# Kernel tuning notes

Measured on AMD Instinct MI355X. Metric: run time of the kernel, lower is better.

Reference implementation:

```python
import jax, jax.numpy as jnp
import numpy as np

N_HEAD = 16
NEG_INF = -1e30  # finite mask value, safe for softmax/grad


def setup_inputs() -> dict:
    key = jax.random.key(0)
    k1, k2, k3 = jax.random.split(key, 3)
    B, T, C = 4, 2049, 1024
    x = jax.random.normal(k1, (B, T, C), dtype=jnp.float32)
    W_attn = jax.random.normal(k2, (C, 3 * C), dtype=jnp.float32) * (1.0 / np.sqrt(C))
    W_proj = jax.random.normal(k3, (C, C), dtype=jnp.float32) * (1.0 / np.sqrt(C))
    return {"x": x, "W_attn": W_attn, "W_proj": W_proj}


def reference(x, W_attn, W_proj):
    B, T, C = x.shape
    H = N_HEAD
    D = C // H
    qkv = x @ W_attn                                  # (B, T, 3C)
    q, k, v = jnp.split(qkv, 3, axis=-1)
    q = q.reshape(B, T, H, D).transpose(0, 2, 1, 3)   # (B, H, T, D)
    k = k.reshape(B, T, H, D).transpose(0, 2, 1, 3)
    v = v.reshape(B, T, H, D).transpose(0, 2, 1, 3)
    # hybrid mask: causal tril, but state token (row 0) attends to ALL positions
    mask = jnp.tril(jnp.ones((T, T), dtype=bool))
    mask = mask.at[0, :].set(True)
    scale = 1.0 / np.sqrt(D)
    scores = jnp.einsum('bhtd,bhsd->bhts', q, k) * scale
    scores = jnp.where(mask[None, None, :, :], scores, NEG_INF)
    att = jax.nn.softmax(scores, axis=-1)
    y = jnp.einsum('bhts,bhsd->bhtd', att, v)         # (B, H, T, D)
    y = y.transpose(0, 2, 1, 3).reshape(B, T, C)
    return y @ W_proj
```

## Files before the change

### kernel.cpp

```cpp
#include <hip/hip_runtime.h>

typedef __attribute__((ext_vector_type(8))) __bf16 bf16x8;
typedef __attribute__((ext_vector_type(4))) __bf16 bf16x4;
typedef __attribute__((ext_vector_type(4))) float f32x4;
typedef __attribute__((ext_vector_type(16))) float f32x16;

#define GLDS(g, l) __builtin_amdgcn_global_load_lds( \
    (__attribute__((address_space(1))) void*)(void*)(g), \
    (__attribute__((address_space(3))) void*)(void*)(l), 16, 0, 0)

constexpr int T_REAL = 2049;
constexpr int Tp     = 2112;
constexpr int Mreal  = 8196;
constexpr int Mp     = 8448;
constexpr int GK     = 1024;

constexpr float QSCALE = 0.125f * 1.4426950408889634f;

__global__ __launch_bounds__(256) void cvt_x(const float* __restrict__ x,
                                             __bf16* __restrict__ xb) {
    size_t i = ((size_t)blockIdx.x * 256 + threadIdx.x) * 4;
    float4 v = make_float4(0.f, 0.f, 0.f, 0.f);
    if (i < (size_t)Mreal * GK) v = *(const float4*)(x + i);
    bf16x4 o;
    o.x = (__bf16)v.x; o.y = (__bf16)v.y; o.z = (__bf16)v.z; o.w = (__bf16)v.w;
    *(bf16x4*)(xb + i) = o;
}

__global__ __launch_bounds__(256) void transpose_w(const float* __restrict__ W,
                                                   __bf16* __restrict__ Wt,
                                                   int K, int N) {
    __shared__ float tile[64][65];
    const int n0 = blockIdx.x * 64, k0 = blockIdx.y * 64;
    const int tx = threadIdx.x & 63, ty = threadIdx.x >> 6;
#pragma unroll
    for (int j = 0; j < 16; j++) {
        int rk = ty + j * 4;
        tile[rk][tx] = W[(size_t)(k0 + rk) * N + n0 + tx];
    }
    __syncthreads();
#pragma unroll
    for (int j = 0; j < 16; j++) {
        int rn = ty + j * 4;
        Wt[(size_t)(n0 + rn) * K + k0 + tx] = (__bf16)tile[tx][rn];
    }
}

__global__ __launch_bounds__(256) void transpose_v(const __bf16* __restrict__ v,
                                                   __bf16* __restrict__ vT) {
    __shared__ __bf16 tl[64][72];
    const int bh = blockIdx.y, t0 = blockIdx.x * 64;
    const int tid = threadIdx.x;
    const __bf16* src = v + ((size_t)bh * Tp + t0) * 64;
    {
        const int r = tid >> 3, c = (tid & 7) * 8;
        *(bf16x8*)&tl[r][c]      = *(const bf16x8*)(src + r * 64 + c);
        *(bf16x8*)&tl[r + 32][c] = *(const bf16x8*)(src + (r + 32) * 64 + c);
    }
    __syncthreads();
    __bf16* dst = vT + (size_t)bh * 64 * Tp + t0;
    {
        const int d = tid >> 3, tc = (tid & 7) * 8;
        bf16x8 a, b;
#pragma unroll
        for (int i = 0; i < 8; i++) {
            a[i] = tl[tc + i][d];
            b[i] = tl[tc + i][d + 32];
        }
        *(bf16x8*)(dst + (size_t)d * Tp + tc)        = a;
        *(bf16x8*)(dst + (size_t)(d + 32) * Tp + tc) = b;
    }
}

__global__ __launch_bounds__(512)
void gemm256(const __bf16* __restrict__ A, const __bf16* __restrict__ Bt,
             __bf16* __restrict__ qout, __bf16* __restrict__ kout,
             __bf16* __restrict__ vout) {
    __shared__ __align__(16) __bf16 As[2][16384];
    __shared__ __align__(16) __bf16 Bs[2][16384];

    const int tid = threadIdx.x, lane = tid & 63, w = tid >> 6;
    const int wr = w >> 2, wc = w & 3;
    const int quad = lane >> 4, l15 = lane & 15, l7 = l15 & 7;
    const int m0 = blockIdx.y * 256, n0 = blockIdx.x * 256;

    const int sr = tid >> 3;
    const int sc = ((tid & 7) ^ (sr & 7)) * 8;
    const __bf16* ag = A  + (size_t)(m0 + sr) * GK + sc;
    const __bf16* bg = Bt + (size_t)(n0 + sr) * GK + sc;
    const int ldst = tid * 8;

#define STG_A(T, h) do { const __bf16* s_ = ag + (size_t)(h) * 128 * GK + (T) * 64; \
    GLDS(s_, &As[(T) & 1][(h) * 8192 + ldst]); \
    GLDS(s_ + (size_t)64 * GK, &As[(T) & 1][(h) * 8192 + 4096 + ldst]); } while (0)
#define STG_B(T, h) do { const __bf16* s_ = bg + (size_t)(h) * 128 * GK + (T) * 64; \
    GLDS(s_, &Bs[(T) & 1][(h) * 8192 + ldst]); \
    GLDS(s_ + (size_t)64 * GK, &Bs[(T) & 1][(h) * 8192 + 4096 + ldst]); } while (0)

    f32x4 acc[8][4] = {};
    bf16x8 a[8], b0[4], b1[4];

    STG_A(0, 0); STG_B(0, 1); STG_A(0, 1); STG_B(0, 0); STG_A(1, 0); STG_B(1, 1);
    asm volatile("s_waitcnt vmcnt(4)" ::: "memory");
    __builtin_amdgcn_s_barrier();

    constexpr int NT = GK / 64;

#pragma unroll 1
    for (int T = 0; T < NT; ++T) {
        const int p = T & 1;

#pragma unroll
        for (int f = 0; f < 4; ++f) {
            const int R = f * 32 + wr * 16 + l15;
            a[f * 2 + 0] = *(const bf16x8*)&As[p][R * 64 + ((quad ^ l7) * 8)];
            a[f * 2 + 1] = *(const bf16x8*)&As[p][R * 64 + (((4 + quad) ^ l7) * 8)];
        }
#pragma unroll
        for (int n = 0; n < 2; ++n) {
            const int R = n * 64 + wc * 16 + l15;
            b0[n * 2 + 0] = *(const bf16x8*)&Bs[p][R * 64 + ((quad ^ l7) * 8)];
            b0[n * 2 + 1] = *(const bf16x8*)&Bs[p][R * 64 + (((4 + quad) ^ l7) * 8)];
        }
        if (T + 1 < NT) { STG_A(T + 1, 1); STG_B(T + 1, 0); }
        __builtin_amdgcn_s_barrier();
        asm volatile("s_waitcnt lgkmcnt(0)" ::: "memory");
        __builtin_amdgcn_sched_barrier(0);
        __builtin_amdgcn_s_setprio(1);
#pragma unroll
        for (int f = 0; f < 4; ++f)
#pragma unroll
            for (int n = 0; n < 2; ++n) {
                acc[f][n] = __builtin_amdgcn_mfma_f32_16x16x32_bf16(a[f*2+0], b0[n*2+0], acc[f][n], 0, 0, 0);
                acc[f][n] = __builtin_amdgcn_mfma_f32_16x16x32_bf16(a[f*2+1], b0[n*2+1], acc[f][n], 0, 0, 0);
            }
        __builtin_amdgcn_s_setprio(0);
        __builtin_amdgcn_s_barrier();

#pragma unroll
        for (int n = 0; n < 2; ++n) {
            const int R = 128 + n * 64 + wc * 16 + l15;
            b1[n * 2 + 0] = *(const bf16x8*)&Bs[p][R * 64 + ((quad ^ l7) * 8)];
            b1[n * 2 + 1] = *(const bf16x8*)&Bs[p][R * 64 + (((4 + quad) ^ l7) * 8)];
        }
        __builtin_amdgcn_s_barrier();
        asm volatile("s_waitcnt lgkmcnt(0)" ::: "memory");
        __builtin_amdgcn_sched_barrier(0);
        __builtin_amdgcn_s_setprio(1);
#pragma unroll
        for (int f = 0; f < 4; ++f)
#pragma unroll
            for (int n = 0; n < 2; ++n) {
                acc[f][2+n] = __builtin_amdgcn_mfma_f32_16x16x32_bf16(a[f*2+0], b1[n*2+0], acc[f][2+n], 0, 0, 0);
                acc[f][2+n] = __builtin_amdgcn_mfma_f32_16x16x32_bf16(a[f*2+1], b1[n*2+1], acc[f][2+n], 0, 0, 0);
            }
        __builtin_amdgcn_s_setprio(0);
        __builtin_amdgcn_s_barrier();

#pragma unroll
        for (int f = 0; f < 4; ++f) {
            const int R = 128 + f * 32 + wr * 16 + l15;
            a[f * 2 + 0] = *(const bf16x8*)&As[p][R * 64 + ((quad ^ l7) * 8)];
            a[f * 2 + 1] = *(const bf16x8*)&As[p][R * 64 + (((4 + quad) ^ l7) * 8)];
        }
        if (T + 2 < NT) STG_A(T + 2, 0);
        __builtin_amdgcn_s_barrier();
        asm volatile("s_waitcnt lgkmcnt(0)" ::: "memory");
        __builtin_amdgcn_sched_barrier(0);
        __builtin_amdgcn_s_setprio(1);
#pragma unroll
        for (int f = 0; f < 4; ++f)
#pragma unroll
            for (int n = 0; n < 2; ++n) {
                acc[4+f][2+n] = __builtin_amdgcn_mfma_f32_16x16x32_bf16(a[f*2+0], b1[n*2+0], acc[4+f][2+n], 0, 0, 0);
                acc[4+f][2+n] = __builtin_amdgcn_mfma_f32_16x16x32_bf16(a[f*2+1], b1[n*2+1], acc[4+f][2+n], 0, 0, 0);
            }
        __builtin_amdgcn_s_setprio(0);
        __builtin_amdgcn_s_barrier();

        if (T + 2 < NT) STG_B(T + 2, 1);
        __builtin_amdgcn_s_barrier();
        asm volatile("s_waitcnt lgkmcnt(0)" ::: "memory");
        __builtin_amdgcn_sched_barrier(0);
        __builtin_amdgcn_s_setprio(1);
#pragma unroll
        for (int f = 0; f < 4; ++f)
#pragma unroll
            for (int n = 0; n < 2; ++n) {
                acc[4+f][n] = __builtin_amdgcn_mfma_f32_16x16x32_bf16(a[f*2+0], b0[n*2+0], acc[4+f][n], 0, 0, 0);
                acc[4+f][n] = __builtin_amdgcn_mfma_f32_16x16x32_bf16(a[f*2+1], b0[n*2+1], acc[4+f][n], 0, 0, 0);
            }
        __builtin_amdgcn_s_setprio(0);
        if (T < NT - 2) { asm volatile("s_waitcnt vmcnt(4)" ::: "memory"); }
        else            { asm volatile("s_waitcnt vmcnt(0)" ::: "memory"); }
        __builtin_amdgcn_s_barrier();
    }
#undef STG_A
#undef STG_B

    const int which = n0 >> 10;
    __bf16* op = (which == 0) ? qout : (which == 1) ? kout : vout;
    const float scl = (which == 0) ? QSCALE : 1.0f;
    __bf16* ep = &As[0][0];
    const int rr = tid >> 4, cc = tid & 15;
#pragma unroll
    for (int f = 0; f < 8; ++f) {
        __syncthreads();
#pragma unroll
        for (int n = 0; n < 4; ++n) {
            const int col = (n & 1) * 64 + wc * 16 + (n >> 1) * 128 + l15;
#pragma unroll
            for (int r = 0; r < 4; ++r)
                ep[(wr * 16 + quad * 4 + r) * 264 + col] = (__bf16)(acc[f][n][r] * scl);
        }
        __syncthreads();
        const int m = m0 + (f & 3) * 32 + (f >> 2) * 128 + rr;
        if (m < Mreal) {
            const int b = m / T_REAL;
            const int t = m - b * T_REAL;
#pragma unroll
            for (int g = 0; g < 2; ++g) {
                const int c8 = (cc + g * 16) * 8;
                bf16x8 vv = *(const bf16x8*)&ep[rr * 264 + c8];
                const int gc = n0 + c8;
                const int h = (gc >> 6) & 15;
                *(bf16x8*)&op[((size_t)(b * 16 + h) * Tp + t) * 64 + (gc & 63)] = vv;
            }
        }
    }
}

template <int EPI>
__global__ __launch_bounds__(256)
void gemm128(const __bf16* __restrict__ A, const __bf16* __restrict__ Bt,
             float* __restrict__ outp,
             __bf16* __restrict__ qout, __bf16* __restrict__ kout,
             __bf16* __restrict__ vout) {
    __shared__ __bf16 As[128 * 64];
    __shared__ __bf16 Bs[128 * 64];

    const int tid = threadIdx.x, lane = tid & 63, w = tid >> 6;
    const int wr = w >> 1, wc = w & 1;
    const int quad = lane >> 4, l15 = lane & 15, l7 = l15 & 7;
    const int m0 = blockIdx.y * 128, n0 = blockIdx.x * 128;

    const int row0 = w * 32 + (lane >> 3);
    const int gc8 = ((lane & 7) ^ ((lane >> 3) & 7)) * 8;
    const __bf16* agp = A + (size_t)(m0 + row0) * GK + gc8;
    const __bf16* bgp = Bt + (size_t)(n0 + row0) * GK + gc8;
    __bf16* lap = &As[(w * 256 + lane) * 8];
    __bf16* lbp = &Bs[(w * 256 + lane) * 8];

    f32x4 acc[4][4] = {};

    for (int k0 = 0; k0 < GK; k0 += 64) {
#pragma unroll
        for (int s = 0; s < 4; s++) {
            GLDS(agp + (size_t)s * 8 * GK + k0, lap + s * 512);
            GLDS(bgp + (size_t)s * 8 * GK + k0, lbp + s * 512);
        }
        __syncthreads();
#pragma unroll
        for (int kk = 0; kk < 2; kk++) {
            bf16x8 fa[4], fb[4];
#pragma unroll
            for (int i = 0; i < 4; i++)
                fa[i] = *(const bf16x8*)&As[(wr * 64 + i * 16 + l15) * 64 + (((kk * 4 + quad) ^ l7) * 8)];
#pragma unroll
            for (int j = 0; j < 4; j++)
                fb[j] = *(const bf16x8*)&Bs[(wc * 64 + j * 16 + l15) * 64 + (((kk * 4 + quad) ^ l7) * 8)];
#pragma unroll
            for (int i = 0; i < 4; i++)
#pragma unroll
                for (int j = 0; j < 4; j++)
                    acc[i][j] = __builtin_amdgcn_mfma_f32_16x16x32_bf16(fa[i], fb[j], acc[i][j], 0, 0, 0);
        }
        __syncthreads();
    }

    if constexpr (EPI == 0) {
        const int which = n0 >> 10;
        const int h = ((n0 + wc * 64) >> 6) & 15;
        __bf16* op = (which == 0) ? qout : (which == 1) ? kout : vout;
        const float scl = (which == 0) ? QSCALE : 1.0f;
        __bf16* wls = &As[w * 2048];
#pragma unroll
        for (int p = 0; p < 2; p++) {
            if (p) __syncthreads();
#pragma unroll
            for (int i2 = 0; i2 < 2; i2++)
#pragma unroll
                for (int j = 0; j < 4; j++)
#pragma unroll
                    for (int r = 0; r < 4; r++) {
                        const int lrow = i2 * 16 + quad * 4 + r;
                        const int cX = (j * 2 + (l15 >> 3)) ^ (lrow & 7);
                        wls[lrow * 64 + cX * 8 + (l15 & 7)] =
                            (__bf16)(acc[p * 2 + i2][j][r] * scl);
                    }
            __syncthreads();
#pragma unroll
            for (int it = 0; it < 4; it++) {
                const int lrow = (lane >> 3) + it * 8;
                bf16x8 vv = *(const bf16x8*)&wls[lrow * 64 + (((lane & 7) ^ (lrow & 7)) * 8)];
                const int m = m0 + wr * 64 + p * 32 + lrow;
                if (m < Mreal) {
                    const int b = m / T_REAL;
                    const int t = m - b * T_REAL;
                    *(bf16x8*)&op[(((size_t)(b * 16 + h)) * Tp + t) * 64 + (lane & 7) * 8] = vv;
                }
            }
        }
    } else {
        float* wlf = (float*)&As[0] + w * 1024;
#pragma unroll
        for (int p = 0; p < 4; p++) {
            if (p) __syncthreads();
#pragma unroll
            for (int j = 0; j < 4; j++)
#pragma unroll
                for (int r = 0; r < 4; r++) {
                    const int lrow = quad * 4 + r;
                    const int cX = (j * 4 + (l15 >> 2)) ^ (lrow & 7);
                    wlf[lrow * 64 + cX * 4 + (l15 & 3)] = acc[p][j][r];
                }
            __syncthreads();
#pragma unroll
            for (int it = 0; it < 4; it++) {
                const int lrow = lane >> 2;
                const int c = (lane & 3) + it * 4;
                f32x4 vv = *(const f32x4*)&wlf[lrow * 64 + ((c ^ (lrow & 7)) * 4)];
                const int m = m0 + wr * 64 + p * 16 + lrow;
                if (m < Mreal)
                    *(f32x4*)&outp[(size_t)m * 1024 + n0 + wc * 64 + c * 4] = vv;
            }
        }
    }
}

__global__ __launch_bounds__(256, 4)
void attn(const __bf16* __restrict__ q, const __bf16* __restrict__ kk,
          const __bf16* __restrict__ vT, __bf16* __restrict__ y) {
    __shared__ __bf16 Ks[2][64 * 64];
    __shared__ __bf16 Vs[2][64 * 64];

    static const int QA[17] = {0,31,29,27,25,23,21,19,17,15,13,11,9,7,5,3,1};
    static const int QB[17] = {32,30,28,26,24,22,20,18,16,14,12,10,8,6,4,2,-1};

    const int tid = threadIdx.x, lane = tid & 63, w = tid >> 6;
    const int l31 = lane & 31, hi = lane >> 5, l7 = l31 & 7;
    const int z = blockIdx.x;
    const int slot = z >> 6, zz = z & 63;
    const int bh = (zz & 7) * 8 + (zz >> 3);

    const int qtA = QA[slot];
    const int qt = (w < 2) ? qtA : QB[slot];
    const bool active = qt >= 0;
    const int qts = active ? qt : 0;
    const int qg = qts * 64 + (w & 1) * 32 + l31;
    const int myNt = (qts == 0) ? 32 : qts;
    const int ntmaxB = (qtA == 0) ? 32 : qtA;

    const __bf16* kgb = kk + (size_t)bh * Tp * 64;
    const __bf16* vgb = vT + (size_t)bh * 64 * Tp;
    const int b = bh >> 4, h = bh & 15;

    const int sr = lane >> 3;
    const int scol = ((lane & 7) ^ sr) * 8;
    const int rk = w * 16 + sr;
    const int ldk = w * 1024 + lane * 8;

    bf16x8 qa[4];
    {
        const __bf16* qp = q + ((size_t)bh * Tp + qg) * 64 + hi * 8;
#pragma unroll
        for (int s = 0; s < 4; ++s) qa[s] = *(const bf16x8*)(qp + s * 16);
    }

    f32x16 o0 = {}, o1 = {};
    float mrow = -3e38f, lrow = 0.f;

    GLDS(kgb + rk * 64 + scol,               &Ks[0][ldk]);
    GLDS(kgb + (rk + 8) * 64 + scol,         &Ks[0][ldk + 512]);
    GLDS(vgb + (size_t)rk * Tp + scol,       &Vs[0][ldk]);
    GLDS(vgb + (size_t)(rk + 8) * Tp + scol, &Vs[0][ldk + 512]);

    int cur = 0;
    for (int nt = 0; nt <= ntmaxB; ++nt) {
        __syncthreads();
        if (nt < ntmaxB) {
            const size_t ko = (size_t)(nt + 1) * 4096;
            const size_t vo = (size_t)(nt + 1) * 64;
            GLDS(kgb + ko + rk * 64 + scol,               &Ks[cur ^ 1][ldk]);
            GLDS(kgb + ko + (rk + 8) * 64 + scol,         &Ks[cur ^ 1][ldk + 512]);
            GLDS(vgb + vo + (size_t)rk * Tp + scol,       &Vs[cur ^ 1][ldk]);
            GLDS(vgb + vo + (size_t)(rk + 8) * Tp + scol, &Vs[cur ^ 1][ldk + 512]);
        }
        if (active && nt <= myNt) {
            const int kv0 = nt * 64;

            f32x16 s0 = {}, s1 = {};
#pragma unroll
            for (int sl = 0; sl < 4; ++sl) {
                const int ch = ((sl * 2 + hi) ^ l7) * 8;
                bf16x8 k0 = *(const bf16x8*)&Ks[cur][l31 * 64 + ch];
                bf16x8 k1 = *(const bf16x8*)&Ks[cur][(32 + l31) * 64 + ch];
                s0 = __builtin_amdgcn_mfma_f32_32x32x16_bf16(k0, qa[sl], s0, 0, 0, 0);
                s1 = __builtin_amdgcn_mfma_f32_32x32x16_bf16(k1, qa[sl], s1, 0, 0, 0);
            }

            if (nt >= qts) {
#pragma unroll
                for (int t = 0; t < 16; ++t) {
                    const int kvg = kv0 + (t & 3) + 8 * (t >> 2) + 4 * hi;
                    const bool v0 = (kvg <= qg) || (qg == 0 && kvg < T_REAL);
                    const bool v1 = (kvg + 32 <= qg) || (qg == 0 && kvg + 32 < T_REAL);
                    s0[t] = v0 ? s0[t] : -1e30f;
                    s1[t] = v1 ? s1[t] : -1e30f;
                }
            }

            float mx = -3e38f;
#pragma unroll
            for (int t = 0; t < 16; ++t) {
                mx = fmaxf(mx, s0[t]);
                mx = fmaxf(mx, s1[t]);
            }
            mx = fmaxf(mx, __shfl_xor(mx, 32));
            if (!__all(mx - mrow <= 8.0f)) {
                const float mn = fmaxf(mrow, mx);
                const float alpha = __builtin_amdgcn_exp2f(mrow - mn);
                mrow = mn;
                lrow *= alpha;
#pragma unroll
                for (int t = 0; t < 16; ++t) { o0[t] *= alpha; o1[t] *= alpha; }
            }

            float rs = 0.f;
#pragma unroll
            for (int t = 0; t < 16; ++t) {
                s0[t] = __builtin_amdgcn_exp2f(s0[t] - mrow);
                s1[t] = __builtin_amdgcn_exp2f(s1[t] - mrow);
                rs += s0[t] + s1[t];
            }
            rs += __shfl_xor(rs, 32);
            lrow += rs;

#pragma unroll
            for (int m = 0; m < 4; ++m) {
                const f32x16 sb = (m & 2) ? s1 : s0;
                constexpr int SB8[4] = {0, 8, 0, 8};
                const int s8 = SB8[m];
                unsigned a01, a23, a45, a67;
                asm("v_cvt_pk_bf16_f32 %0, %1, %2" : "=v"(a01) : "v"(sb[s8 + 0]), "v"(sb[s8 + 1]));
                asm("v_cvt_pk_bf16_f32 %0, %1, %2" : "=v"(a23) : "v"(sb[s8 + 2]), "v"(sb[s8 + 3]));
                asm("v_cvt_pk_bf16_f32 %0, %1, %2" : "=v"(a45) : "v"(sb[s8 + 4]), "v"(sb[s8 + 5]));
                asm("v_cvt_pk_bf16_f32 %0, %1, %2" : "=v"(a67) : "v"(sb[s8 + 6]), "v"(sb[s8 + 7]));
                asm("v_permlane32_swap_b32 %0, %1" : "+v"(a01), "+v"(a45));
                asm("v_permlane32_swap_b32 %0, %1" : "+v"(a23), "+v"(a67));
                union { unsigned u[4]; bf16x8 v; } pf;
                pf.u[0] = a01; pf.u[1] = a23; pf.u[2] = a45; pf.u[3] = a67;
                const int ch = ((m * 2 + hi) ^ l7) * 8;
                bf16x8 v0 = *(const bf16x8*)&Vs[cur][l31 * 64 + ch];
                bf16x8 v1 = *(const bf16x8*)&Vs[cur][(32 + l31) * 64 + ch];
                o0 = __builtin_amdgcn_mfma_f32_32x32x16_bf16(v0, pf.v, o0, 0, 0, 0);
                o1 = __builtin_amdgcn_mfma_f32_32x32x16_bf16(v1, pf.v, o1, 0, 0, 0);
            }
        }
        cur ^= 1;
    }

    if (active && qg < T_REAL) {
        const float inv = 1.0f / lrow;
        __bf16* yp = y + ((size_t)(b * T_REAL + qg)) * 1024 + h * 64 + hi * 4;
#pragma unroll
        for (int g = 0; g < 4; ++g) {
            bf16x4 w0, w1;
            w0.x = (__bf16)(o0[g * 4 + 0] * inv);
            w0.y = (__bf16)(o0[g * 4 + 1] * inv);
            w0.z = (__bf16)(o0[g * 4 + 2] * inv);
            w0.w = (__bf16)(o0[g * 4 + 3] * inv);
            w1.x = (__bf16)(o1[g * 4 + 0] * inv);
            w1.y = (__bf16)(o1[g * 4 + 1] * inv);
            w1.z = (__bf16)(o1[g * 4 + 2] * inv);
            w1.w = (__bf16)(o1[g * 4 + 3] * inv);
            *(bf16x4*)(yp + g * 8)      = w0;
            *(bf16x4*)(yp + 32 + g * 8) = w1;
        }
    }
}

extern "C" void kernel_launch(void* const* d_in, const int* in_sizes, int n_in,
                              void* d_out, int out_size, void* d_ws, size_t ws_size,
                              hipStream_t stream) {
    const float* x  = (const float*)d_in[0];
    const float* Wa = (const float*)d_in[1];
    const float* Wp = (const float*)d_in[2];
    float* out = (float*)d_out;

    char* ws = (char*)d_ws;
    constexpr size_t SZ_XB  = (size_t)Mp * GK * 2;
    constexpr size_t SZ_WAT = (size_t)3072 * GK * 2;
    constexpr size_t SZ_WPT = (size_t)1024 * GK * 2;
    constexpr size_t SZ_QK  = (size_t)64 * Tp * 64 * 2;
    __bf16* xb   = (__bf16*)(ws);
    __bf16* WaT  = (__bf16*)(ws + SZ_XB);
    __bf16* WpT  = (__bf16*)(ws + SZ_XB + SZ_WAT);
    __bf16* qb   = (__bf16*)(ws + SZ_XB + SZ_WAT + SZ_WPT);
    __bf16* kb   = (__bf16*)(ws + SZ_XB + SZ_WAT + SZ_WPT + SZ_QK);
    __bf16* vTb  = (__bf16*)(ws + SZ_XB + SZ_WAT + SZ_WPT + 2 * SZ_QK);
    __bf16* shrd = (__bf16*)(ws + SZ_XB + SZ_WAT + SZ_WPT + 3 * SZ_QK);
    __bf16* vpre = shrd;
    __bf16* yb   = shrd;

    cvt_x<<<(Mp * GK) / 1024, 256, 0, stream>>>(x, xb);
    transpose_w<<<dim3(48, 16), 256, 0, stream>>>(Wa, WaT, 1024, 3072);
    transpose_w<<<dim3(16, 16), 256, 0, stream>>>(Wp, WpT, 1024, 1024);

    gemm256<<<dim3(12, 33), 512, 0, stream>>>(xb, WaT, qb, kb, vpre);
    transpose_v<<<dim3(33, 64), 256, 0, stream>>>(vpre, vTb);
    attn<<<1088, 256, 0, stream>>>(qb, kb, vTb, yb);
    gemm128<1><<<dim3(8, 65), 256, 0, stream>>>(yb, WpT, out, nullptr, nullptr, nullptr);
}
```

Measured before the change: 277.1 us.

## Fuse prep kernels into one launch and write V transposed from GEMM epilogue

Merges the x conversion and both weight transposes into a single prep kernel dispatched by block index. The QKV GEMM now writes the V part directly in transposed (d-major) layout from registers, which removes the separate transpose_v kernel and the intermediate V buffer round trip. This saves two launches plus a global read and write of V. In exchange the V stores become strided 8-byte writes along t, which may coalesce poorly.

After: 284.2 us. +2.6%, slower.

```diff
diff --git a/kernel.cpp b/kernel.cpp
--- a/kernel.cpp
+++ b/kernel.cpp
@@ -17,21 +17,26 @@
 
 constexpr float QSCALE = 0.125f * 1.4426950408889634f;
 
-__global__ __launch_bounds__(256) void cvt_x(const float* __restrict__ x,
-                                             __bf16* __restrict__ xb) {
-    size_t i = ((size_t)blockIdx.x * 256 + threadIdx.x) * 4;
-    float4 v = make_float4(0.f, 0.f, 0.f, 0.f);
-    if (i < (size_t)Mreal * GK) v = *(const float4*)(x + i);
-    bf16x4 o;
-    o.x = (__bf16)v.x; o.y = (__bf16)v.y; o.z = (__bf16)v.z; o.w = (__bf16)v.w;
-    *(bf16x4*)(xb + i) = o;
-}
-
-__global__ __launch_bounds__(256) void transpose_w(const float* __restrict__ W,
-                                                   __bf16* __restrict__ Wt,
-                                                   int K, int N) {
+__global__ __launch_bounds__(256)
+void prep(const float* __restrict__ x, __bf16* __restrict__ xb,
+          const float* __restrict__ Wa, __bf16* __restrict__ WaT,
+          const float* __restrict__ Wp, __bf16* __restrict__ WpT) {
     __shared__ float tile[64][65];
-    const int n0 = blockIdx.x * 64, k0 = blockIdx.y * 64;
+    const int z = blockIdx.x;
+    if (z < 8448) {
+        size_t i = ((size_t)z * 256 + threadIdx.x) * 4;
+        float4 v = make_float4(0.f, 0.f, 0.f, 0.f);
+        if (i < (size_t)Mreal * GK) v = *(const float4*)(x + i);
+        bf16x4 o;
+        o.x = (__bf16)v.x; o.y = (__bf16)v.y; o.z = (__bf16)v.z; o.w = (__bf16)v.w;
+        *(bf16x4*)(xb + i) = o;
+        return;
+    }
+    const float* W; __bf16* Wt; int N, idx;
+    if (z < 9216) { W = Wa; Wt = WaT; N = 3072; idx = z - 8448; }
+    else          { W = Wp; Wt = WpT; N = 1024; idx = z - 9216; }
+    const int ntiles = N >> 6;
+    const int n0 = (idx % ntiles) * 64, k0 = (idx / ntiles) * 64;
     const int tx = threadIdx.x & 63, ty = threadIdx.x >> 6;
 #pragma unroll
     for (int j = 0; j < 16; j++) {
@@ -42,33 +47,7 @@
 #pragma unroll
     for (int j = 0; j < 16; j++) {
         int rn = ty + j * 4;
-        Wt[(size_t)(n0 + rn) * K + k0 + tx] = (__bf16)tile[tx][rn];
-    }
-}
-
-__global__ __launch_bounds__(256) void transpose_v(const __bf16* __restrict__ v,
-                                                   __bf16* __restrict__ vT) {
-    __shared__ __bf16 tl[64][72];
-    const int bh = blockIdx.y, t0 = blockIdx.x * 64;
-    const int tid = threadIdx.x;
-    const __bf16* src = v + ((size_t)bh * Tp + t0) * 64;
-    {
-        const int r = tid >> 3, c = (tid & 7) * 8;
-        *(bf16x8*)&tl[r][c]      = *(const bf16x8*)(src + r * 64 + c);
-        *(bf16x8*)&tl[r + 32][c] = *(const bf16x8*)(src + (r + 32) * 64 + c);
-    }
-    __syncthreads();
-    __bf16* dst = vT + (size_t)bh * 64 * Tp + t0;
-    {
-        const int d = tid >> 3, tc = (tid & 7) * 8;
-        bf16x8 a, b;
-#pragma unroll
-        for (int i = 0; i < 8; i++) {
-            a[i] = tl[tc + i][d];
-            b[i] = tl[tc + i][d + 32];
-        }
-        *(bf16x8*)(dst + (size_t)d * Tp + tc)        = a;
-        *(bf16x8*)(dst + (size_t)(d + 32) * Tp + tc) = b;
+        Wt[(size_t)(n0 + rn) * GK + k0 + tx] = (__bf16)tile[tx][rn];
     }
 }
 
@@ -199,7 +178,42 @@
 #undef STG_B
 
     const int which = n0 >> 10;
-    __bf16* op = (which == 0) ? qout : (which == 1) ? kout : vout;
+
+    if (which == 2) {
+#pragma unroll
+        for (int f = 0; f < 8; ++f) {
+            const int mb = m0 + (f & 3) * 32 + (f >> 2) * 128 + wr * 16 + quad * 4;
+#pragma unroll
+            for (int n = 0; n < 4; ++n) {
+                const int c = (n0 - 2048) + (n & 1) * 64 + wc * 16 + (n >> 1) * 128 + l15;
+                const int hh = c >> 6, d = c & 63;
+                const int bA = mb / T_REAL, bB = (mb + 3) / T_REAL;
+                if (bA == bB && mb + 3 < Mreal) {
+                    const int t = mb - bA * T_REAL;
+                    bf16x4 vv;
+                    vv.x = (__bf16)acc[f][n][0];
+                    vv.y = (__bf16)acc[f][n][1];
+                    vv.z = (__bf16)acc[f][n][2];
+                    vv.w = (__bf16)acc[f][n][3];
+                    *(bf16x4*)&vout[(size_t)(bA * 16 + hh) * 64 * Tp + (size_t)d * Tp + t] = vv;
+                } else {
+#pragma unroll
+                    for (int r = 0; r < 4; ++r) {
+                        const int m = mb + r;
+                        if (m < Mreal) {
+                            const int bb = m / T_REAL;
+                            const int t = m - bb * T_REAL;
+                            vout[(size_t)(bb * 16 + hh) * 64 * Tp + (size_t)d * Tp + t] =
+                                (__bf16)acc[f][n][r];
+                        }
+                    }
+                }
+            }
+        }
+        return;
+    }
+
+    __bf16* op = (which == 0) ? qout : kout;
     const float scl = (which == 0) ? QSCALE : 1.0f;
     __bf16* ep = &As[0][0];
     const int rr = tid >> 4, cc = tid & 15;
@@ -509,16 +523,10 @@
     __bf16* qb   = (__bf16*)(ws + SZ_XB + SZ_WAT + SZ_WPT);
     __bf16* kb   = (__bf16*)(ws + SZ_XB + SZ_WAT + SZ_WPT + SZ_QK);
     __bf16* vTb  = (__bf16*)(ws + SZ_XB + SZ_WAT + SZ_WPT + 2 * SZ_QK);
-    __bf16* shrd = (__bf16*)(ws + SZ_XB + SZ_WAT + SZ_WPT + 3 * SZ_QK);
-    __bf16* vpre = shrd;
-    __bf16* yb   = shrd;
-
-    cvt_x<<<(Mp * GK) / 1024, 256, 0, stream>>>(x, xb);
-    transpose_w<<<dim3(48, 16), 256, 0, stream>>>(Wa, WaT, 1024, 3072);
-    transpose_w<<<dim3(16, 16), 256, 0, stream>>>(Wp, WpT, 1024, 1024);
-
-    gemm256<<<dim3(12, 33), 512, 0, stream>>>(xb, WaT, qb, kb, vpre);
-    transpose_v<<<dim3(33, 64), 256, 0, stream>>>(vpre, vTb);
+    __bf16* yb   = (__bf16*)(ws + SZ_XB + SZ_WAT + SZ_WPT + 3 * SZ_QK);
+
+    prep<<<9472, 256, 0, stream>>>(x, xb, Wa, WaT, Wp, WpT);
+    gemm256<<<dim3(12, 33), 512, 0, stream>>>(xb, WaT, qb, kb, vTb);
     attn<<<1088, 256, 0, stream>>>(qb, kb, vTb, yb);
     gemm128<1><<<dim3(8, 65), 256, 0, stream>>>(yb, WpT, out, nullptr, nullptr, nullptr);
 }
```

## Process 64 query rows per wave in attention and fuse prep kernels

Applied to the files above, without the earlier changes.

The attention kernel drops from 4 waves to 2 waves per block, and each wave now computes two 32-row query groups against the same K/V fragments it reads from LDS. This halves LDS reads per MFMA and reuses the K and V register loads across both query groups. The cost is roughly doubled accumulator and score registers, which lowers occupancy (launch bounds go from 256,4 to 128,2). Separately, the x conversion and the two weight transposes are merged into one prep launch to cut launch overhead.

Result: slower. 290.7 us (+4.9%).

```diff
diff --git a/kernel.cpp b/kernel.cpp
--- a/kernel.cpp
+++ b/kernel.cpp
@@ -17,21 +17,26 @@
 
 constexpr float QSCALE = 0.125f * 1.4426950408889634f;
 
-__global__ __launch_bounds__(256) void cvt_x(const float* __restrict__ x,
-                                             __bf16* __restrict__ xb) {
-    size_t i = ((size_t)blockIdx.x * 256 + threadIdx.x) * 4;
-    float4 v = make_float4(0.f, 0.f, 0.f, 0.f);
-    if (i < (size_t)Mreal * GK) v = *(const float4*)(x + i);
-    bf16x4 o;
-    o.x = (__bf16)v.x; o.y = (__bf16)v.y; o.z = (__bf16)v.z; o.w = (__bf16)v.w;
-    *(bf16x4*)(xb + i) = o;
-}
-
-__global__ __launch_bounds__(256) void transpose_w(const float* __restrict__ W,
-                                                   __bf16* __restrict__ Wt,
-                                                   int K, int N) {
+__global__ __launch_bounds__(256)
+void prep(const float* __restrict__ x, __bf16* __restrict__ xb,
+          const float* __restrict__ Wa, __bf16* __restrict__ WaT,
+          const float* __restrict__ Wp, __bf16* __restrict__ WpT) {
     __shared__ float tile[64][65];
-    const int n0 = blockIdx.x * 64, k0 = blockIdx.y * 64;
+    const int z = blockIdx.x;
+    if (z < 8448) {
+        size_t i = ((size_t)z * 256 + threadIdx.x) * 4;
+        float4 v = make_float4(0.f, 0.f, 0.f, 0.f);
+        if (i < (size_t)Mreal * GK) v = *(const float4*)(x + i);
+        bf16x4 o;
+        o.x = (__bf16)v.x; o.y = (__bf16)v.y; o.z = (__bf16)v.z; o.w = (__bf16)v.w;
+        *(bf16x4*)(xb + i) = o;
+        return;
+    }
+    const float* W; __bf16* Wt; int N, idx;
+    if (z < 9216) { W = Wa; Wt = WaT; N = 3072; idx = z - 8448; }
+    else          { W = Wp; Wt = WpT; N = 1024; idx = z - 9216; }
+    const int ntiles = N >> 6;
+    const int n0 = (idx % ntiles) * 64, k0 = (idx / ntiles) * 64;
     const int tx = threadIdx.x & 63, ty = threadIdx.x >> 6;
 #pragma unroll
     for (int j = 0; j < 16; j++) {
@@ -42,7 +47,7 @@
 #pragma unroll
     for (int j = 0; j < 16; j++) {
         int rn = ty + j * 4;
-        Wt[(size_t)(n0 + rn) * K + k0 + tx] = (__bf16)tile[tx][rn];
+        Wt[(size_t)(n0 + rn) * GK + k0 + tx] = (__bf16)tile[tx][rn];
     }
 }
 
@@ -338,7 +343,7 @@
     }
 }
 
-__global__ __launch_bounds__(256, 4)
+__global__ __launch_bounds__(128, 2)
 void attn(const __bf16* __restrict__ q, const __bf16* __restrict__ kk,
           const __bf16* __restrict__ vT, __bf16* __restrict__ y) {
     __shared__ __bf16 Ks[2][64 * 64];
@@ -354,10 +359,11 @@
     const int bh = (zz & 7) * 8 + (zz >> 3);
 
     const int qtA = QA[slot];
-    const int qt = (w < 2) ? qtA : QB[slot];
+    const int qt = (w == 0) ? qtA : QB[slot];
     const bool active = qt >= 0;
     const int qts = active ? qt : 0;
-    const int qg = qts * 64 + (w & 1) * 32 + l31;
+    const int qgA = qts * 64 + l31;
+    const int qgB = qts * 64 + 32 + l31;
     const int myNt = (qts == 0) ? 32 : qts;
     const int ntmaxB = (qtA == 0) ? 32 : qtA;
 
@@ -365,25 +371,30 @@
     const __bf16* vgb = vT + (size_t)bh * 64 * Tp;
     const int b = bh >> 4, h = bh & 15;
 
-    const int sr = lane >> 3;
-    const int scol = ((lane & 7) ^ sr) * 8;
-    const int rk = w * 16 + sr;
-    const int ldk = w * 1024 + lane * 8;
-
-    bf16x8 qa[4];
+    const int sr8 = lane >> 3;
+    const int scol = ((lane & 7) ^ sr8) * 8;
+    const int rk = w * 32 + sr8;
+    const int ldk = w * 2048 + lane * 8;
+
+    bf16x8 qaA[4], qaB[4];
     {
-        const __bf16* qp = q + ((size_t)bh * Tp + qg) * 64 + hi * 8;
-#pragma unroll
-        for (int s = 0; s < 4; ++s) qa[s] = *(const bf16x8*)(qp + s * 16);
-    }
-
-    f32x16 o0 = {}, o1 = {};
-    float mrow = -3e38f, lrow = 0.f;
-
-    GLDS(kgb + rk * 64 + scol,               &Ks[0][ldk]);
-    GLDS(kgb + (rk + 8) * 64 + scol,         &Ks[0][ldk + 512]);
-    GLDS(vgb + (size_t)rk * Tp + scol,       &Vs[0][ldk]);
-    GLDS(vgb + (size_t)(rk + 8) * Tp + scol, &Vs[0][ldk + 512]);
+        const __bf16* qpA = q + ((size_t)bh * Tp + qgA) * 64 + hi * 8;
+        const __bf16* qpB = q + ((size_t)bh * Tp + qgB) * 64 + hi * 8;
+#pragma unroll
+        for (int s = 0; s < 4; ++s) {
+            qaA[s] = *(const bf16x8*)(qpA + s * 16);
+            qaB[s] = *(const bf16x8*)(qpB + s * 16);
+        }
+    }
+
+    f32x16 oA0 = {}, oA1 = {}, oB0 = {}, oB1 = {};
+    float mrowA = -3e38f, lrowA = 0.f, mrowB = -3e38f, lrowB = 0.f;
+
+#pragma unroll
+    for (int g = 0; g < 4; ++g) {
+        GLDS(kgb + (rk + 8 * g) * 64 + scol,         &Ks[0][ldk + 512 * g]);
+        GLDS(vgb + (size_t)(rk + 8 * g) * Tp + scol, &Vs[0][ldk + 512 * g]);
+    }
 
     int cur = 0;
     for (int nt = 0; nt <= ntmaxB; ++nt) {
@@ -391,99 +402,153 @@
         if (nt < ntmaxB) {
             const size_t ko = (size_t)(nt + 1) * 4096;
             const size_t vo = (size_t)(nt + 1) * 64;
-            GLDS(kgb + ko + rk * 64 + scol,               &Ks[cur ^ 1][ldk]);
-            GLDS(kgb + ko + (rk + 8) * 64 + scol,         &Ks[cur ^ 1][ldk + 512]);
-            GLDS(vgb + vo + (size_t)rk * Tp + scol,       &Vs[cur ^ 1][ldk]);
-            GLDS(vgb + vo + (size_t)(rk + 8) * Tp + scol, &Vs[cur ^ 1][ldk + 512]);
+#pragma unroll
+            for (int g = 0; g < 4; ++g) {
+                GLDS(kgb + ko + (rk + 8 * g) * 64 + scol,         &Ks[cur ^ 1][ldk + 512 * g]);
+                GLDS(vgb + vo + (size_t)(rk + 8 * g) * Tp + scol, &Vs[cur ^ 1][ldk + 512 * g]);
+            }
         }
         if (active && nt <= myNt) {
             const int kv0 = nt * 64;
 
-            f32x16 s0 = {}, s1 = {};
+            f32x16 sA0 = {}, sA1 = {}, sB0 = {}, sB1 = {};
 #pragma unroll
             for (int sl = 0; sl < 4; ++sl) {
                 const int ch = ((sl * 2 + hi) ^ l7) * 8;
                 bf16x8 k0 = *(const bf16x8*)&Ks[cur][l31 * 64 + ch];
                 bf16x8 k1 = *(const bf16x8*)&Ks[cur][(32 + l31) * 64 + ch];
-                s0 = __builtin_amdgcn_mfma_f32_32x32x16_bf16(k0, qa[sl], s0, 0, 0, 0);
-                s1 = __builtin_amdgcn_mfma_f32_32x32x16_bf16(k1, qa[sl], s1, 0, 0, 0);
+                sA0 = __builtin_amdgcn_mfma_f32_32x32x16_bf16(k0, qaA[sl], sA0, 0, 0, 0);
+                sA1 = __builtin_amdgcn_mfma_f32_32x32x16_bf16(k1, qaA[sl], sA1, 0, 0, 0);
+                sB0 = __builtin_amdgcn_mfma_f32_32x32x16_bf16(k0, qaB[sl], sB0, 0, 0, 0);
+                sB1 = __builtin_amdgcn_mfma_f32_32x32x16_bf16(k1, qaB[sl], sB1, 0, 0, 0);
             }
 
             if (nt >= qts) {
 #pragma unroll
                 for (int t = 0; t < 16; ++t) {
                     const int kvg = kv0 + (t & 3) + 8 * (t >> 2) + 4 * hi;
-                    const bool v0 = (kvg <= qg) || (qg == 0 && kvg < T_REAL);
-                    const bool v1 = (kvg + 32 <= qg) || (qg == 0 && kvg + 32 < T_REAL);
-                    s0[t] = v0 ? s0[t] : -1e30f;
-                    s1[t] = v1 ? s1[t] : -1e30f;
-                }
-            }
-
-            float mx = -3e38f;
-#pragma unroll
-            for (int t = 0; t < 16; ++t) {
-                mx = fmaxf(mx, s0[t]);
-                mx = fmaxf(mx, s1[t]);
-            }
-            mx = fmaxf(mx, __shfl_xor(mx, 32));
-            if (!__all(mx - mrow <= 8.0f)) {
-                const float mn = fmaxf(mrow, mx);
-                const float alpha = __builtin_amdgcn_exp2f(mrow - mn);
-                mrow = mn;
-                lrow *= alpha;
-#pragma unroll
-                for (int t = 0; t < 16; ++t) { o0[t] *= alpha; o1[t] *= alpha; }
-            }
-
-            float rs = 0.f;
-#pragma unroll
-            for (int t = 0; t < 16; ++t) {
-                s0[t] = __builtin_amdgcn_exp2f(s0[t] - mrow);
-                s1[t] = __builtin_amdgcn_exp2f(s1[t] - mrow);
-                rs += s0[t] + s1[t];
-            }
-            rs += __shfl_xor(rs, 32);
-            lrow += rs;
+                    const bool a0 = (kvg <= qgA) || (qgA == 0 && kvg < T_REAL);
+                    const bool a1 = (kvg + 32 <= qgA) || (qgA == 0 && kvg + 32 < T_REAL);
+                    sA0[t] = a0 ? sA0[t] : -1e30f;
+                    sA1[t] = a1 ? sA1[t] : -1e30f;
+                    const bool b0v = (kvg <= qgB);
+                    const bool b1v = (kvg + 32 <= qgB);
+                    sB0[t] = b0v ? sB0[t] : -1e30f;
+                    sB1[t] = b1v ? sB1[t] : -1e30f;
+                }
+            }
+
+            {
+                float mx = -3e38f;
+#pragma unroll
+                for (int t = 0; t < 16; ++t) { mx = fmaxf(mx, sA0[t]); mx = fmaxf(mx, sA1[t]); }
+                mx = fmaxf(mx, __shfl_xor(mx, 32));
+                if (!__all(mx - mrowA <= 8.0f)) {
+                    const float mn = fmaxf(mrowA, mx);
+                    const float alpha = __builtin_amdgcn_exp2f(mrowA - mn);
+                    mrowA = mn; lrowA *= alpha;
+#pragma unroll
+                    for (int t = 0; t < 16; ++t) { oA0[t] *= alpha; oA1[t] *= alpha; }
+                }
+                float rs = 0.f;
+#pragma unroll
+                for (int t = 0; t < 16; ++t) {
+                    sA0[t] = __builtin_amdgcn_exp2f(sA0[t] - mrowA);
+                    sA1[t] = __builtin_amdgcn_exp2f(sA1[t] - mrowA);
+                    rs += sA0[t] + sA1[t];
+                }
+                rs += __shfl_xor(rs, 32);
+                lrowA += rs;
+            }
+            {
+                float mx = -3e38f;
+#pragma unroll
+                for (int t = 0; t < 16; ++t) { mx = fmaxf(mx, sB0[t]); mx = fmaxf(mx, sB1[t]); }
+                mx = fmaxf(mx, __shfl_xor(mx, 32));
+                if (!__all(mx - mrowB <= 8.0f)) {
+                    const float mn = fmaxf(mrowB, mx);
+                    const float alpha = __builtin_amdgcn_exp2f(mrowB - mn);
+                    mrowB = mn; lrowB *= alpha;
+#pragma unroll
+                    for (int t = 0; t < 16; ++t) { oB0[t] *= alpha; oB1[t] *= alpha; }
+                }
+                float rs = 0.f;
+#pragma unroll
+                for (int t = 0; t < 16; ++t) {
+                    sB0[t] = __builtin_amdgcn_exp2f(sB0[t] - mrowB);
+                    sB1[t] = __builtin_amdgcn_exp2f(sB1[t] - mrowB);
+                    rs += sB0[t] + sB1[t];
+                }
+                rs += __shfl_xor(rs, 32);
+                lrowB += rs;
+            }
 
 #pragma unroll
             for (int m = 0; m < 4; ++m) {
-                const f32x16 sb = (m & 2) ? s1 : s0;
                 constexpr int SB8[4] = {0, 8, 0, 8};
                 const int s8 = SB8[m];
-                unsigned a01, a23, a45, a67;
-                asm("v_cvt_pk_bf16_f32 %0, %1, %2" : "=v"(a01) : "v"(sb[s8 + 0]), "v"(sb[s8 + 1]));
-                asm("v_cvt_pk_bf16_f32 %0, %1, %2" : "=v"(a23) : "v"(sb[s8 + 2]), "v"(sb[s8 + 3]));
-                asm("v_cvt_pk_bf16_f32 %0, %1, %2" : "=v"(a45) : "v"(sb[s8 + 4]), "v"(sb[s8 + 5]));
-                asm("v_cvt_pk_bf16_f32 %0, %1, %2" : "=v"(a67) : "v"(sb[s8 + 6]), "v"(sb[s8 + 7]));
+                const f32x16 sa = (m & 2) ? sA1 : sA0;
+                const f32x16 sb = (m & 2) ? sB1 : sB0;
+                unsigned a01, a23, a45, a67, c01, c23, c45, c67;
+                asm("v_cvt_pk_bf16_f32 %0, %1, %2" : "=v"(a01) : "v"(sa[s8 + 0]), "v"(sa[s8 + 1]));
+                asm("v_cvt_pk_bf16_f32 %0, %1, %2" : "=v"(a23) : "v"(sa[s8 + 2]), "v"(sa[s8 + 3]));
+                asm("v_cvt_pk_bf16_f32 %0, %1, %2" : "=v"(a45) : "v"(sa[s8 + 4]), "v"(sa[s8 + 5]));
+                asm("v_cvt_pk_bf16_f32 %0, %1, %2" : "=v"(a67) : "v"(sa[s8 + 6]), "v"(sa[s8 + 7]));
                 asm("v_permlane32_swap_b32 %0, %1" : "+v"(a01), "+v"(a45));
                 asm("v_permlane32_swap_b32 %0, %1" : "+v"(a23), "+v"(a67));
-                union { unsigned u[4]; bf16x8 v; } pf;
-                pf.u[0] = a01; pf.u[1] = a23; pf.u[2] = a45; pf.u[3] = a67;
+                asm("v_cvt_pk_bf16_f32 %0, %1, %2" : "=v"(c01) : "v"(sb[s8 + 0]), "v"(sb[s8 + 1]));
+                asm("v_cvt_pk_bf16_f32 %0, %1, %2" : "=v"(c23) : "v"(sb[s8 + 2]), "v"(sb[s8 + 3]));
+                asm("v_cvt_pk_bf16_f32 %0, %1, %2" : "=v"(c45) : "v"(sb[s8 + 4]), "v"(sb[s8 + 5]));
+                asm("v_cvt_pk_bf16_f32 %0, %1, %2" : "=v"(c67) : "v"(sb[s8 + 6]), "v"(sb[s8 + 7]));
+                asm("v_permlane32_swap_b32 %0, %1" : "+v"(c01), "+v"(c45));
+                asm("v_permlane32_swap_b32 %0, %1" : "+v"(c23), "+v"(c67));
+                union { unsigned u[4]; bf16x8 v; } pfA, pfB;
+                pfA.u[0] = a01; pfA.u[1] = a23; pfA.u[2] = a45; pfA.u[3] = a67;
+                pfB.u[0] = c01; pfB.u[1] = c23; pfB.u[2] = c45; pfB.u[3] = c67;
                 const int ch = ((m * 2 + hi) ^ l7) * 8;
                 bf16x8 v0 = *(const bf16x8*)&Vs[cur][l31 * 64 + ch];
                 bf16x8 v1 = *(const bf16x8*)&Vs[cur][(32 + l31) * 64 + ch];
-                o0 = __builtin_amdgcn_mfma_f32_32x32x16_bf16(v0, pf.v, o0, 0, 0, 0);
-                o1 = __builtin_amdgcn_mfma_f32_32x32x16_bf16(v1, pf.v, o1, 0, 0, 0);
+                oA0 = __builtin_amdgcn_mfma_f32_32x32x16_bf16(v0, pfA.v, oA0, 0, 0, 0);
+                oA1 = __builtin_amdgcn_mfma_f32_32x32x16_bf16(v1, pfA.v, oA1, 0, 0, 0);
+                oB0 = __builtin_amdgcn_mfma_f32_32x32x16_bf16(v0, pfB.v, oB0, 0, 0, 0);
+                oB1 = __builtin_amdgcn_mfma_f32_32x32x16_bf16(v1, pfB.v, oB1, 0, 0, 0);
             }
         }
         cur ^= 1;
     }
 
-    if (active && qg < T_REAL) {
-        const float inv = 1.0f / lrow;
-        __bf16* yp = y + ((size_t)(b * T_REAL + qg)) * 1024 + h * 64 + hi * 4;
+    if (active && qgA < T_REAL) {
+        const float inv = 1.0f / lrowA;
+        __bf16* yp = y + ((size_t)(b * T_REAL + qgA)) * 1024 + h * 64 + hi * 4;
 #pragma unroll
         for (int g = 0; g < 4; ++g) {
             bf16x4 w0, w1;
-            w0.x = (__bf16)(o0[g * 4 + 0] * inv);
-            w0.y = (__bf16)(o0[g * 4 + 1] * inv);
-            w0.z = (__bf16)(o0[g * 4 + 2] * inv);
-            w0.w = (__bf16)(o0[g * 4 + 3] * inv);
-            w1.x = (__bf16)(o1[g * 4 + 0] * inv);
-            w1.y = (__bf16)(o1[g * 4 + 1] * inv);
-            w1.z = (__bf16)(o1[g * 4 + 2] * inv);
-            w1.w = (__bf16)(o1[g * 4 + 3] * inv);
+            w0.x = (__bf16)(oA0[g * 4 + 0] * inv);
+            w0.y = (__bf16)(oA0[g * 4 + 1] * inv);
+            w0.z = (__bf16)(oA0[g * 4 + 2] * inv);
+            w0.w = (__bf16)(oA0[g * 4 + 3] * inv);
+            w1.x = (__bf16)(oA1[g * 4 + 0] * inv);
+            w1.y = (__bf16)(oA1[g * 4 + 1] * inv);
+            w1.z = (__bf16)(oA1[g * 4 + 2] * inv);
+            w1.w = (__bf16)(oA1[g * 4 + 3] * inv);
+            *(bf16x4*)(yp + g * 8)      = w0;
+            *(bf16x4*)(yp + 32 + g * 8) = w1;
+        }
+    }
+    if (active && qgB < T_REAL) {
+        const float inv = 1.0f / lrowB;
+        __bf16* yp = y + ((size_t)(b * T_REAL + qgB)) * 1024 + h * 64 + hi * 4;
+#pragma unroll
+        for (int g = 0; g < 4; ++g) {
+            bf16x4 w0, w1;
+            w0.x = (__bf16)(oB0[g * 4 + 0] * inv);
+            w0.y = (__bf16)(oB0[g * 4 + 1] * inv);
+            w0.z = (__bf16)(oB0[g * 4 + 2] * inv);
+            w0.w = (__bf16)(oB0[g * 4 + 3] * inv);
+            w1.x = (__bf16)(oB1[g * 4 + 0] * inv);
+            w1.y = (__bf16)(oB1[g * 4 + 1] * inv);
+            w1.z = (__bf16)(oB1[g * 4 + 2] * inv);
+            w1.w = (__bf16)(oB1[g * 4 + 3] * inv);
             *(bf16x4*)(yp + g * 8)      = w0;
             *(bf16x4*)(yp + 32 + g * 8) = w1;
         }
@@ -513,12 +578,9 @@
     __bf16* vpre = shrd;
     __bf16* yb   = shrd;
 
-    cvt_x<<<(Mp * GK) / 1024, 256, 0, stream>>>(x, xb);
-    transpose_w<<<dim3(48, 16), 256, 0, stream>>>(Wa, WaT, 1024, 3072);
-    transpose_w<<<dim3(16, 16), 256, 0, stream>>>(Wp, WpT, 1024, 1024);
-
+    prep<<<9472, 256, 0, stream>>>(x, xb, Wa, WaT, Wp, WpT);
     gemm256<<<dim3(12, 33), 512, 0, stream>>>(xb, WaT, qb, kb, vpre);
     transpose_v<<<dim3(33, 64), 256, 0, stream>>>(vpre, vTb);
-    attn<<<1088, 256, 0, stream>>>(qb, kb, vTb, yb);
+    attn<<<1088, 128, 0, stream>>>(qb, kb, vTb, yb);
     gemm128<1><<<dim3(8, 65), 256, 0, stream>>>(yb, WpT, out, nullptr, nullptr, nullptr);
 }
```

## Merge prep kernels and deepen attention K/V prefetch with explicit vmcnt waits

Applied to the files above, without the earlier changes.

The three preprocessing launches (x conversion and two weight transposes) are merged into one kernel that dispatches on block index, removing two launches. In the attention kernel, K/V tiles are now prefetched two iterations ahead into the double buffer. A partial s_waitcnt vmcnt(4) replaces the full sync-before-issue pattern, with a second barrier before the buffer is refilled. This lets global-to-LDS loads overlap more compute, at the cost of an extra barrier per iteration and reliance on hand-counted outstanding loads.

After: 273.6 us. No clear change (-1.2%).

```diff
diff --git a/kernel.cpp b/kernel.cpp
--- a/kernel.cpp
+++ b/kernel.cpp
@@ -17,21 +17,26 @@
 
 constexpr float QSCALE = 0.125f * 1.4426950408889634f;
 
-__global__ __launch_bounds__(256) void cvt_x(const float* __restrict__ x,
-                                             __bf16* __restrict__ xb) {
-    size_t i = ((size_t)blockIdx.x * 256 + threadIdx.x) * 4;
-    float4 v = make_float4(0.f, 0.f, 0.f, 0.f);
-    if (i < (size_t)Mreal * GK) v = *(const float4*)(x + i);
-    bf16x4 o;
-    o.x = (__bf16)v.x; o.y = (__bf16)v.y; o.z = (__bf16)v.z; o.w = (__bf16)v.w;
-    *(bf16x4*)(xb + i) = o;
-}
-
-__global__ __launch_bounds__(256) void transpose_w(const float* __restrict__ W,
-                                                   __bf16* __restrict__ Wt,
-                                                   int K, int N) {
+__global__ __launch_bounds__(256)
+void prep(const float* __restrict__ x, __bf16* __restrict__ xb,
+          const float* __restrict__ Wa, __bf16* __restrict__ WaT,
+          const float* __restrict__ Wp, __bf16* __restrict__ WpT) {
     __shared__ float tile[64][65];
-    const int n0 = blockIdx.x * 64, k0 = blockIdx.y * 64;
+    const int z = blockIdx.x;
+    if (z < 8448) {
+        size_t i = ((size_t)z * 256 + threadIdx.x) * 4;
+        float4 v = make_float4(0.f, 0.f, 0.f, 0.f);
+        if (i < (size_t)Mreal * GK) v = *(const float4*)(x + i);
+        bf16x4 o;
+        o.x = (__bf16)v.x; o.y = (__bf16)v.y; o.z = (__bf16)v.z; o.w = (__bf16)v.w;
+        *(bf16x4*)(xb + i) = o;
+        return;
+    }
+    const float* W; __bf16* Wt; int N, idx;
+    if (z < 9216) { W = Wa; Wt = WaT; N = 3072; idx = z - 8448; }
+    else          { W = Wp; Wt = WpT; N = 1024; idx = z - 9216; }
+    const int ntiles = N >> 6;
+    const int n0 = (idx % ntiles) * 64, k0 = (idx / ntiles) * 64;
     const int tx = threadIdx.x & 63, ty = threadIdx.x >> 6;
 #pragma unroll
     for (int j = 0; j < 16; j++) {
@@ -42,7 +47,7 @@
 #pragma unroll
     for (int j = 0; j < 16; j++) {
         int rn = ty + j * 4;
-        Wt[(size_t)(n0 + rn) * K + k0 + tx] = (__bf16)tile[tx][rn];
+        Wt[(size_t)(n0 + rn) * GK + k0 + tx] = (__bf16)tile[tx][rn];
     }
 }
 
@@ -380,22 +385,24 @@
     f32x16 o0 = {}, o1 = {};
     float mrow = -3e38f, lrow = 0.f;
 
-    GLDS(kgb + rk * 64 + scol,               &Ks[0][ldk]);
-    GLDS(kgb + (rk + 8) * 64 + scol,         &Ks[0][ldk + 512]);
-    GLDS(vgb + (size_t)rk * Tp + scol,       &Vs[0][ldk]);
-    GLDS(vgb + (size_t)(rk + 8) * Tp + scol, &Vs[0][ldk + 512]);
-
-    int cur = 0;
+#define STG_KV(NT_, BUF_) do { \
+    const size_t ko_ = (size_t)(NT_) * 4096, vo_ = (size_t)(NT_) * 64; \
+    GLDS(kgb + ko_ + rk * 64 + scol,               &Ks[BUF_][ldk]); \
+    GLDS(kgb + ko_ + (rk + 8) * 64 + scol,         &Ks[BUF_][ldk + 512]); \
+    GLDS(vgb + vo_ + (size_t)rk * Tp + scol,       &Vs[BUF_][ldk]); \
+    GLDS(vgb + vo_ + (size_t)(rk + 8) * Tp + scol, &Vs[BUF_][ldk + 512]); } while (0)
+
+    STG_KV(0, 0);
+    STG_KV(1, 1);
+
+#pragma unroll 1
     for (int nt = 0; nt <= ntmaxB; ++nt) {
-        __syncthreads();
-        if (nt < ntmaxB) {
-            const size_t ko = (size_t)(nt + 1) * 4096;
-            const size_t vo = (size_t)(nt + 1) * 64;
-            GLDS(kgb + ko + rk * 64 + scol,               &Ks[cur ^ 1][ldk]);
-            GLDS(kgb + ko + (rk + 8) * 64 + scol,         &Ks[cur ^ 1][ldk + 512]);
-            GLDS(vgb + vo + (size_t)rk * Tp + scol,       &Vs[cur ^ 1][ldk]);
-            GLDS(vgb + vo + (size_t)(rk + 8) * Tp + scol, &Vs[cur ^ 1][ldk + 512]);
-        }
+        const int cur = nt & 1;
+        if (nt < ntmaxB) { asm volatile("s_waitcnt vmcnt(4)" ::: "memory"); }
+        else             { asm volatile("s_waitcnt vmcnt(0)" ::: "memory"); }
+        __builtin_amdgcn_s_barrier();
+        asm volatile("" ::: "memory");
+
         if (active && nt <= myNt) {
             const int kv0 = nt * 64;
 
@@ -467,8 +474,13 @@
                 o1 = __builtin_amdgcn_mfma_f32_32x32x16_bf16(v1, pf.v, o1, 0, 0, 0);
             }
         }
-        cur ^= 1;
-    }
+
+        asm volatile("" ::: "memory");
+        __builtin_amdgcn_s_barrier();
+        asm volatile("" ::: "memory");
+        if (nt + 2 <= ntmaxB) STG_KV(nt + 2, cur);
+    }
+#undef STG_KV
 
     if (active && qg < T_REAL) {
         const float inv = 1.0f / lrow;
@@ -513,10 +525,7 @@
     __bf16* vpre = shrd;
     __bf16* yb   = shrd;
 
-    cvt_x<<<(Mp * GK) / 1024, 256, 0, stream>>>(x, xb);
-    transpose_w<<<dim3(48, 16), 256, 0, stream>>>(Wa, WaT, 1024, 3072);
-    transpose_w<<<dim3(16, 16), 256, 0, stream>>>(Wp, WpT, 1024, 1024);
-
+    prep<<<9472, 256, 0, stream>>>(x, xb, Wa, WaT, Wp, WpT);
     gemm256<<<dim3(12, 33), 512, 0, stream>>>(xb, WaT, qb, kb, vpre);
     transpose_v<<<dim3(33, 64), 256, 0, stream>>>(vpre, vTb);
     attn<<<1088, 256, 0, stream>>>(qb, kb, vTb, yb);
```
